# Optimization experiments

Hardware: AMD Instinct MI355X
Metric: run time of the kernel (lower is better)

The kernel has to match this reference:

```python
import jax, jax.numpy as jnp
import numpy as np

NUM_HEADS = 16
HEAD_DIM = 64  # hidden_size // num_heads = 1024 // 16


def setup_inputs() -> dict:
    key = jax.random.key(0)
    ks = jax.random.split(key, 5)
    B, S, D = 4, 2048, 1024
    scale = 1.0 / np.sqrt(D)
    return {
        "hidden_states": jax.random.normal(ks[0], (B, S, D), dtype=jnp.float32),
        "Wq": jax.random.normal(ks[1], (D, D), dtype=jnp.float32) * scale,
        "Wk": jax.random.normal(ks[2], (D, D), dtype=jnp.float32) * scale,
        "Wv": jax.random.normal(ks[3], (D, D), dtype=jnp.float32) * scale,
        "Wo": jax.random.normal(ks[4], (D, D), dtype=jnp.float32) * scale,
    }


def reference(hidden_states, Wq, Wk, Wv, Wo):
    B, S, D = hidden_states.shape
    H, hd = NUM_HEADS, HEAD_DIM
    # torch nn.Linear(y = x @ W.T), bias=False
    q = (hidden_states @ Wq.T).reshape(B, S, H, hd)
    k = (hidden_states @ Wk.T).reshape(B, S, H, hd)
    v = (hidden_states @ Wv.T).reshape(B, S, H, hd)
    q = q / jnp.sqrt(jnp.float32(hd))
    # scores: [B, H, S, S] — module materializes full score matrix
    scores = jnp.einsum("bqhd,bkhd->bhqk", q, k)
    weights = jax.nn.softmax(scores, axis=-1)
    attn = jnp.einsum("bhqk,bkhd->bqhd", weights, v).reshape(B, S, D)
    return attn @ Wo.T
```

## Files before the change

### kernel.cpp

```cpp
#include <hip/hip_runtime.h>

using u16 = unsigned short;
using u32 = unsigned int;
typedef __attribute__((ext_vector_type(8))) short bf16x8;
typedef __attribute__((ext_vector_type(4))) short bf16x4;
typedef __attribute__((ext_vector_type(4))) float f32x4;
typedef __attribute__((ext_vector_type(16))) float f32x16;
typedef __attribute__((ext_vector_type(4))) u32 u32x4;

__device__ __forceinline__ u16 f2bf(float f) {
  u32 u = __builtin_bit_cast(u32, f);
  u += 0x7FFFu + ((u >> 16) & 1u);
  return (u16)(u >> 16);
}

__device__ __forceinline__ void load_lds16(const void* g, void* l) {
  typedef const __attribute__((address_space(1))) u32 GA;
  typedef __attribute__((address_space(3))) u32 LA;
  __builtin_amdgcn_global_load_lds((GA*)g, (LA*)l, 16, 0, 0);
}

__device__ __forceinline__ bf16x4 tr16(const u16* p) {
  typedef __attribute__((address_space(3))) const u16 LT;
  bf16x4 d;
  asm volatile("ds_read_b64_tr_b16 %0, %1" : "=v"(d) : "v"((LT*)p));
  return d;
}

__device__ __forceinline__ float exp2_fast(float x) {
  float r;
  asm("v_exp_f32 %0, %1" : "=v"(r) : "v"(x));
  return r;
}

__device__ __forceinline__ u32 cvt_pk_bf16(float lo, float hi) {
  u32 r;
  asm("v_cvt_pk_bf16_f32 %0, %1, %2" : "=v"(r) : "v"(lo), "v"(hi));
  return r;
}

__device__ __forceinline__ void permlane32_swap(u32& a, u32& b) {
  asm volatile("v_permlane32_swap_b32 %0, %1" : "+v"(a), "+v"(b));
}

__global__ void cvt_bf16(const float* __restrict__ src, u16* __restrict__ dst,
                         int n4, float scale) {
  int i = blockIdx.x * blockDim.x + threadIdx.x;
  if (i >= n4) return;
  float4 v = reinterpret_cast<const float4*>(src)[i];
  ushort4 o;
  o.x = f2bf(v.x * scale);
  o.y = f2bf(v.y * scale);
  o.z = f2bf(v.z * scale);
  o.w = f2bf(v.w * scale);
  reinterpret_cast<ushort4*>(dst)[i] = o;
}

__global__ void cvt_w4(const float* __restrict__ Wq, const float* __restrict__ Wk,
                       const float* __restrict__ Wv, const float* __restrict__ Wo,
                       u16* __restrict__ dst, int n4seg, float qscale) {
  int i = blockIdx.x * blockDim.x + threadIdx.x;
  int seg = i / n4seg, off = i - seg * n4seg;
  const float* src = seg == 0 ? Wq : seg == 1 ? Wk : seg == 2 ? Wv : Wo;
  float sc = seg == 0 ? qscale : 1.0f;
  float4 v = reinterpret_cast<const float4*>(src)[off];
  ushort4 o;
  o.x = f2bf(v.x * sc);
  o.y = f2bf(v.y * sc);
  o.z = f2bf(v.z * sc);
  o.w = f2bf(v.w * sc);
  reinterpret_cast<ushort4*>(dst)[i] = o;
}

template <int NH>
__device__ __forceinline__ void mq(f32x4 (&acc)[4][4], bf16x8 (&afr)[4][2],
                                   bf16x8 (&bfr)[2][2]) {
  __builtin_amdgcn_s_setprio(1);
#pragma unroll
  for (int m = 0; m < 4; ++m)
#pragma unroll
    for (int n = 0; n < 2; ++n)
#pragma unroll
      for (int ks = 0; ks < 2; ++ks)
        acc[m][NH * 2 + n] = __builtin_amdgcn_mfma_f32_16x16x32_bf16(
            afr[m][ks], bfr[n][ks], acc[m][NH * 2 + n], 0, 0, 0);
  __builtin_amdgcn_s_setprio(0);
}

#define GBAR() __builtin_amdgcn_s_barrier()
#define PW()                                               \
  do {                                                     \
    GBAR();                                                \
    asm volatile("s_waitcnt lgkmcnt(0)" ::: "memory");     \
  } while (0)
#define PWV(N)                                                          \
  do {                                                                  \
    GBAR();                                                             \
    asm volatile("s_waitcnt vmcnt(" #N ") lgkmcnt(0)" ::: "memory");    \
  } while (0)

template <typename OutT>
__global__ __launch_bounds__(512, 2) void gemm256x128(
    const u16* __restrict__ A, const u16* __restrict__ Bw,
    OutT* __restrict__ C, int M, int N, int K) {
  __shared__ __align__(16) char ldsb[98304];
  const int tid = threadIdx.x;
  const int wid = tid >> 6, lane = tid & 63;
  const int wr = wid >> 1, wc = wid & 1;
  const int laneR = lane & 15, laneG = lane >> 4;
  const int swzR = (laneR & 7) << 4;

  const int nbm = M >> 8;
  const int cpx = gridDim.x >> 3;
  const int id = blockIdx.x;
  const int swzid = (id & 7) * cpx + (id >> 3);
  const int bm = swzid % nbm, bn = swzid / nbm;

  const u16* Ab = A + (size_t)(bm * 256) * K;
  const u16* Bb = Bw + (size_t)(bn * 128) * K;

  const int s_r = tid >> 3;
  const int s_k = ((tid & 7) ^ (s_r & 7)) * 8;

  auto stage_unit = [&](const u16* Xb, int dstoff, int row0, int kt) {
    char* d = ldsb + dstoff + wid * 1024;
#pragma unroll
    for (int j = 0; j < 2; ++j)
      load_lds16(Xb + (size_t)(row0 + j * 64 + s_r) * K + kt * 64 + s_k,
                 d + j * 8192);
  };
  auto rdA = [&](int buf, int m, int ks) -> bf16x8 {
    return *(const bf16x8*)(ldsb + buf * 32768 + (wr >> 1) * 16384 +
                            ((wr & 1) * 64 + m * 16 + laneR) * 128 +
                            ((ks * 64 + laneG * 16) ^ swzR));
  };
  auto rdB = [&](int buf, int nh, int n, int ks) -> bf16x8 {
    return *(const bf16x8*)(ldsb + 65536 + buf * 16384 +
                            (wc * 64 + nh * 32 + n * 16 + laneR) * 128 +
                            ((ks * 64 + laneG * 16) ^ swzR));
  };

  f32x4 acc[4][4];
#pragma unroll
  for (int i = 0; i < 4; ++i)
#pragma unroll
    for (int j = 0; j < 4; ++j) acc[i][j] = f32x4{0.f, 0.f, 0.f, 0.f};

  bf16x8 afr[4][2], bfr[2][2];
  auto readA = [&](int buf) {
#pragma unroll
    for (int m = 0; m < 4; ++m) {
      afr[m][0] = rdA(buf, m, 0);
      afr[m][1] = rdA(buf, m, 1);
    }
  };
  auto readB = [&](int buf, int nh) {
#pragma unroll
    for (int n = 0; n < 2; ++n) {
      bfr[n][0] = rdB(buf, nh, n, 0);
      bfr[n][1] = rdB(buf, nh, n, 1);
    }
  };

  const int NT = K >> 6, NI = K >> 7;

  stage_unit(Ab, 0, 0, 0);
  stage_unit(Ab, 16384, 128, 0);
  stage_unit(Bb, 65536, 0, 0);
  stage_unit(Ab, 32768, 0, 1);
  asm volatile("s_waitcnt vmcnt(2)" ::: "memory");
  GBAR();

  for (int i = 0; i < NI; ++i) {
    const int tb = (2 * i + 1) & (NT - 1);
    const int tc = (2 * i + 2) & (NT - 1);
    const int td = (2 * i + 3) & (NT - 1);
    readA(0); readB(0, 0);
    stage_unit(Ab, 32768 + 16384, 128, tb);
    stage_unit(Bb, 65536 + 16384, 0, tb);
    PW();
    mq<0>(acc, afr, bfr); GBAR();
    readB(0, 1);
    stage_unit(Ab, 0, 0, tc);
    stage_unit(Ab, 16384, 128, tc);
    PWV(4);
    mq<1>(acc, afr, bfr); GBAR();
    readA(1); readB(1, 0);
    stage_unit(Bb, 65536, 0, tc);
    PW();
    mq<0>(acc, afr, bfr); GBAR();
    readB(1, 1);
    stage_unit(Ab, 32768, 0, td);
    PWV(2);
    mq<1>(acc, afr, bfr); GBAR();
  }

  const int crow = bm * 256 + wr * 64;
  const int ccol = bn * 128 + wc * 64;
#pragma unroll
  for (int mf = 0; mf < 4; ++mf)
#pragma unroll
    for (int nf = 0; nf < 4; ++nf)
#pragma unroll
      for (int r = 0; r < 4; ++r) {
        int row = crow + mf * 16 + laneG * 4 + r;
        int col = ccol + nf * 16 + laneR;
        float v = acc[mf][nf][r];
        if constexpr (sizeof(OutT) == 2)
          C[(size_t)row * N + col] = f2bf(v);
        else
          C[(size_t)row * N + col] = v;
      }
}

__global__ __launch_bounds__(512, 4) void flash_attn(
    const u16* __restrict__ QKV, u16* __restrict__ O) {
  constexpr int S = 2048, DQ = 3072, DO = 1024;
  __shared__ u16 Kt[2][4096];
  __shared__ u16 Vt[2][4096];
  const int tid = threadIdx.x, wid = tid >> 6, lane = tid & 63;
  const int lq = lane & 31, hi = lane >> 5;

  const int id = blockIdx.x;
  const int jj0 = id >> 3;
  const int bh = (id & 7) * 8 + (jj0 >> 3), qt = jj0 & 7;
  const int b = bh >> 4, h = bh & 15;

  const size_t bq = (size_t)b * S * DQ;
  const u16* Qg = QKV + bq + h * 64;
  const u16* Kg = QKV + bq + 1024 + h * 64;
  const u16* Vg = QKV + bq + 2048 + h * 64;
  const int qrow0 = qt * 256 + wid * 32;

  const int k_kv = tid >> 3;
  const int k_col = ((tid & 7) ^ (k_kv & 7)) * 8;
  const int v_kv = ((tid >> 5) << 2) | ((tid >> 1) & 3);
  const int v_hd = (((tid >> 3) & 3) << 4) | ((tid & 1) << 3);

  bf16x8 qf[4];
#pragma unroll
  for (int kc = 0; kc < 4; ++kc)
    qf[kc] = *(const bf16x8*)&Qg[(size_t)(qrow0 + lq) * DQ + kc * 16 + hi * 8];

  f32x16 o0, o1;
#pragma unroll
  for (int r = 0; r < 16; ++r) { o0[r] = 0.f; o1[r] = 0.f; }
  float l = 0.f;

  auto stage = [&](int buf, int kv0) {
    load_lds16(Kg + (size_t)(kv0 + k_kv) * DQ + k_col, &Kt[buf][wid * 512]);
    load_lds16(Vg + (size_t)(kv0 + v_kv) * DQ + v_hd, &Vt[buf][wid * 512]);
  };

  stage(0, 0);
  __syncthreads();

  for (int t = 0; t < 32; ++t) {
    const int cur = t & 1;
    stage(cur ^ 1, ((t + 1) & 31) * 64);

    f32x16 st[2];
#pragma unroll
    for (int blk = 0; blk < 2; ++blk) {
#pragma unroll
      for (int r = 0; r < 16; ++r) st[blk][r] = 0.f;
      bf16x8 kf[4];
#pragma unroll
      for (int kc = 0; kc < 4; ++kc) {
        int kv = blk * 32 + lq;
        int byt = kv * 128 + ((kc * 32 + hi * 16) ^ ((kv & 7) << 4));
        kf[kc] = *(const bf16x8*)((const char*)&Kt[cur][0] + byt);
      }
      __builtin_amdgcn_s_setprio(1);
#pragma unroll
      for (int kc = 0; kc < 4; ++kc)
        st[blk] = __builtin_amdgcn_mfma_f32_32x32x16_bf16(kf[kc], qf[kc], st[blk], 0, 0, 0);
      __builtin_amdgcn_s_setprio(0);
    }

    float ps = 0.f;
#pragma unroll
    for (int blk = 0; blk < 2; ++blk)
#pragma unroll
      for (int r = 0; r < 16; ++r) {
        float p = exp2_fast(st[blk][r]);
        st[blk][r] = p;
        ps += p;
      }
    l += ps;

    u32 W0[8], W1[8];
#pragma unroll
    for (int r2 = 0; r2 < 8; ++r2) {
      W0[r2] = cvt_pk_bf16(st[0][2 * r2], st[0][2 * r2 + 1]);
      W1[r2] = cvt_pk_bf16(st[1][2 * r2], st[1][2 * r2 + 1]);
    }
    bf16x8 pb[4];
#pragma unroll
    for (int ks = 0; ks < 2; ++ks) {
      u32 a0 = W0[4 * ks], a2 = W0[4 * ks + 2];
      u32 a1 = W0[4 * ks + 1], a3 = W0[4 * ks + 3];
      permlane32_swap(a0, a2);
      permlane32_swap(a1, a3);
      pb[ks] = __builtin_bit_cast(bf16x8, u32x4{a0, a1, a2, a3});
    }
#pragma unroll
    for (int ks = 0; ks < 2; ++ks) {
      u32 a0 = W1[4 * ks], a2 = W1[4 * ks + 2];
      u32 a1 = W1[4 * ks + 1], a3 = W1[4 * ks + 3];
      permlane32_swap(a0, a2);
      permlane32_swap(a1, a3);
      pb[2 + ks] = __builtin_bit_cast(bf16x8, u32x4{a0, a1, a2, a3});
    }

#pragma unroll
    for (int c2 = 0; c2 < 2; ++c2) {
      bf16x4 vh[4][2];
      const int hb = c2 * 2 + ((lane >> 4) & 1);
#pragma unroll
      for (int ks = 0; ks < 4; ++ks)
#pragma unroll
        for (int p2 = 0; p2 < 2; ++p2) {
          int a = ks * 4 + hi * 2 + p2;
          vh[ks][p2] = tr16(&Vt[cur][(a * 4 + hb) * 64 + (lane & 15) * 4]);
        }
      asm volatile("s_waitcnt lgkmcnt(0)" ::: "memory");
      __builtin_amdgcn_sched_barrier(0);
      __builtin_amdgcn_s_setprio(1);
      f32x16 oc = c2 ? o1 : o0;
#pragma unroll
      for (int ks = 0; ks < 4; ++ks) {
        bf16x8 vf = __builtin_shufflevector(vh[ks][0], vh[ks][1], 0, 1, 2, 3, 4, 5, 6, 7);
        oc = __builtin_amdgcn_mfma_f32_32x32x16_bf16(vf, pb[ks], oc, 0, 0, 0);
      }
      if (c2) o1 = oc; else o0 = oc;
      __builtin_amdgcn_s_setprio(0);
    }

    __syncthreads();
  }

  l += __shfl_xor(l, 32);
  const float inv = 1.0f / l;
  const size_t boo = (size_t)b * S * DO + h * 64;
  const size_t qb = boo + (size_t)(qrow0 + lq) * DO;
#pragma unroll
  for (int r = 0; r < 16; ++r) {
    int hd = (r & 3) + 8 * (r >> 2) + 4 * hi;
    O[qb + hd] = f2bf(o0[r] * inv);
    O[qb + 32 + hd] = f2bf(o1[r] * inv);
  }
}

extern "C" void kernel_launch(void* const* d_in, const int* in_sizes, int n_in,
                              void* d_out, int out_size, void* d_ws, size_t ws_size,
                              hipStream_t stream) {
  const float* hs = (const float*)d_in[0];
  const float* Wq = (const float*)d_in[1];
  const float* Wk = (const float*)d_in[2];
  const float* Wv = (const float*)d_in[3];
  const float* Wo = (const float*)d_in[4];
  float* out = (float*)d_out;

  constexpr int Bn = 4, S = 2048, Dm = 1024;
  constexpr int M = Bn * S;
  constexpr size_t SZ = (size_t)M * Dm;
  constexpr size_t WSZ = (size_t)Dm * Dm;

  u16* wsp = (u16*)d_ws;
  u16* QKVb = wsp;
  u16* hs16 = QKVb + (size_t)M * 3072;
  u16* Ob = hs16;
  u16* W16 = hs16 + SZ;
  u16* Wo16 = W16 + 3 * WSZ;
  (void)ws_size; (void)in_sizes; (void)n_in; (void)out_size;

  cvt_bf16<<<(int)(SZ / 4 / 256), 256, 0, stream>>>(hs, hs16, (int)(SZ / 4), 1.0f);
  cvt_w4<<<(int)(4 * WSZ / 4 / 256), 256, 0, stream>>>(
      Wq, Wk, Wv, Wo, W16, (int)(WSZ / 4), 0.125f * 1.44269504f);

  gemm256x128<u16><<<(M / 256) * (3072 / 128), 512, 0, stream>>>(hs16, W16, QKVb, M, 3072, Dm);

  flash_attn<<<512, 512, 0, stream>>>(QKVb, Ob);

  gemm256x128<float><<<(M / 256) * (Dm / 128), 512, 0, stream>>>(Ob, Wo16, out, M, Dm, Dm);
}
```

Measured before the change: 197.1 us.

## Fuse conversion kernels, chunk GEMM tile order, triple-buffer attention K/V

Merges the activation and weight bf16 conversion kernels into one launch. Remaps GEMM block IDs into row/column chunks for better L2 reuse. The attention kernel moves from double- to triple-buffered K/V staging with prefetch two tiles ahead, waiting on vmcnt instead of a full syncthreads. It also seeds the first MFMA with a zero accumulator and drops the setprio hints. In exchange it uses more LDS per block and adds some scheduling risk.

```diff
diff --git a/kernel.cpp b/kernel.cpp
--- a/kernel.cpp
+++ b/kernel.cpp
@@ -43,34 +43,50 @@
   asm volatile("v_permlane32_swap_b32 %0, %1" : "+v"(a), "+v"(b));
 }
 
-__global__ void cvt_bf16(const float* __restrict__ src, u16* __restrict__ dst,
-                         int n4, float scale) {
+__global__ void cvt_all(const float* __restrict__ hs, const float* __restrict__ Wq,
+                        const float* __restrict__ Wk, const float* __restrict__ Wv,
+                        const float* __restrict__ Wo, u16* __restrict__ hs16,
+                        u16* __restrict__ w16, int hs4, int w4seg, float qscale) {
   int i = blockIdx.x * blockDim.x + threadIdx.x;
-  if (i >= n4) return;
-  float4 v = reinterpret_cast<const float4*>(src)[i];
-  ushort4 o;
-  o.x = f2bf(v.x * scale);
-  o.y = f2bf(v.y * scale);
-  o.z = f2bf(v.z * scale);
-  o.w = f2bf(v.w * scale);
-  reinterpret_cast<ushort4*>(dst)[i] = o;
-}
-
-__global__ void cvt_w4(const float* __restrict__ Wq, const float* __restrict__ Wk,
-                       const float* __restrict__ Wv, const float* __restrict__ Wo,
-                       u16* __restrict__ dst, int n4seg, float qscale) {
-  int i = blockIdx.x * blockDim.x + threadIdx.x;
-  int seg = i / n4seg, off = i - seg * n4seg;
-  const float* src = seg == 0 ? Wq : seg == 1 ? Wk : seg == 2 ? Wv : Wo;
-  float sc = seg == 0 ? qscale : 1.0f;
+  const float* src;
+  u16* dst;
+  float sc = 1.0f;
+  int off;
+  if (i < hs4) {
+    src = hs; dst = hs16; off = i;
+  } else {
+    int j = i - hs4;
+    int seg = j / w4seg;
+    off = j - seg * w4seg;
+    dst = w16 + (size_t)seg * (size_t)w4seg * 4;
+    src = seg == 0 ? Wq : seg == 1 ? Wk : seg == 2 ? Wv : Wo;
+    if (seg == 0) sc = qscale;
+  }
   float4 v = reinterpret_cast<const float4*>(src)[off];
   ushort4 o;
   o.x = f2bf(v.x * sc);
   o.y = f2bf(v.y * sc);
   o.z = f2bf(v.z * sc);
   o.w = f2bf(v.w * sc);
-  reinterpret_cast<ushort4*>(dst)[i] = o;
-}
+  reinterpret_cast<ushort4*>(dst)[off] = o;
+}
+
+#define GBAR() __builtin_amdgcn_s_barrier()
+#define PWAIT()                                            \
+  do {                                                     \
+    GBAR();                                                \
+    asm volatile("s_waitcnt lgkmcnt(0)" ::: "memory");     \
+  } while (0)
+#define PWAITV()                                                    \
+  do {                                                              \
+    GBAR();                                                         \
+    asm volatile("s_waitcnt vmcnt(2) lgkmcnt(0)" ::: "memory");     \
+  } while (0)
+#define PWAITV4()                                                   \
+  do {                                                              \
+    GBAR();                                                         \
+    asm volatile("s_waitcnt vmcnt(4) lgkmcnt(0)" ::: "memory");     \
+  } while (0)
 
 template <int NH>
 __device__ __forceinline__ void mq(f32x4 (&acc)[4][4], bf16x8 (&afr)[4][2],
@@ -87,22 +103,10 @@
   __builtin_amdgcn_s_setprio(0);
 }
 
-#define GBAR() __builtin_amdgcn_s_barrier()
-#define PW()                                               \
-  do {                                                     \
-    GBAR();                                                \
-    asm volatile("s_waitcnt lgkmcnt(0)" ::: "memory");     \
-  } while (0)
-#define PWV(N)                                                          \
-  do {                                                                  \
-    GBAR();                                                             \
-    asm volatile("s_waitcnt vmcnt(" #N ") lgkmcnt(0)" ::: "memory");    \
-  } while (0)
-
 template <typename OutT>
 __global__ __launch_bounds__(512, 2) void gemm256x128(
     const u16* __restrict__ A, const u16* __restrict__ Bw,
-    OutT* __restrict__ C, int M, int N, int K) {
+    OutT* __restrict__ C, int M, int N, int K, int rpc, int nbnc) {
   __shared__ __align__(16) char ldsb[98304];
   const int tid = threadIdx.x;
   const int wid = tid >> 6, lane = tid & 63;
@@ -110,11 +114,15 @@
   const int laneR = lane & 15, laneG = lane >> 4;
   const int swzR = (laneR & 7) << 4;
 
-  const int nbm = M >> 8;
+  const int nbn = N >> 7;
   const int cpx = gridDim.x >> 3;
   const int id = blockIdx.x;
   const int swzid = (id & 7) * cpx + (id >> 3);
-  const int bm = swzid % nbm, bn = swzid / nbm;
+  const int c = swzid / cpx, j = swzid % cpx;
+  const int ncc = nbn / nbnc;
+  const int chunk_row = c / ncc, chunk_col = c % ncc;
+  const int bm = chunk_row * rpc + j / nbnc;
+  const int bn = chunk_col * nbnc + j % nbnc;
 
   const u16* Ab = A + (size_t)(bm * 256) * K;
   const u16* Bb = Bw + (size_t)(bn * 128) * K;
@@ -125,9 +133,9 @@
   auto stage_unit = [&](const u16* Xb, int dstoff, int row0, int kt) {
     char* d = ldsb + dstoff + wid * 1024;
 #pragma unroll
-    for (int j = 0; j < 2; ++j)
-      load_lds16(Xb + (size_t)(row0 + j * 64 + s_r) * K + kt * 64 + s_k,
-                 d + j * 8192);
+    for (int jj = 0; jj < 2; ++jj)
+      load_lds16(Xb + (size_t)(row0 + jj * 64 + s_r) * K + kt * 64 + s_k,
+                 d + jj * 8192);
   };
   auto rdA = [&](int buf, int m, int ks) -> bf16x8 {
     return *(const bf16x8*)(ldsb + buf * 32768 + (wr >> 1) * 16384 +
@@ -144,7 +152,7 @@
 #pragma unroll
   for (int i = 0; i < 4; ++i)
 #pragma unroll
-    for (int j = 0; j < 4; ++j) acc[i][j] = f32x4{0.f, 0.f, 0.f, 0.f};
+    for (int jj = 0; jj < 4; ++jj) acc[i][jj] = f32x4{0.f, 0.f, 0.f, 0.f};
 
   bf16x8 afr[4][2], bfr[2][2];
   auto readA = [&](int buf) {
@@ -178,20 +186,20 @@
     readA(0); readB(0, 0);
     stage_unit(Ab, 32768 + 16384, 128, tb);
     stage_unit(Bb, 65536 + 16384, 0, tb);
-    PW();
+    PWAIT();
     mq<0>(acc, afr, bfr); GBAR();
     readB(0, 1);
     stage_unit(Ab, 0, 0, tc);
     stage_unit(Ab, 16384, 128, tc);
-    PWV(4);
+    PWAITV4();
     mq<1>(acc, afr, bfr); GBAR();
     readA(1); readB(1, 0);
     stage_unit(Bb, 65536, 0, tc);
-    PW();
+    PWAIT();
     mq<0>(acc, afr, bfr); GBAR();
     readB(1, 1);
     stage_unit(Ab, 32768, 0, td);
-    PWV(2);
+    PWAITV();
     mq<1>(acc, afr, bfr); GBAR();
   }
 
@@ -216,8 +224,8 @@
 __global__ __launch_bounds__(512, 4) void flash_attn(
     const u16* __restrict__ QKV, u16* __restrict__ O) {
   constexpr int S = 2048, DQ = 3072, DO = 1024;
-  __shared__ u16 Kt[2][4096];
-  __shared__ u16 Vt[2][4096];
+  __shared__ u16 Kt[3][4096];
+  __shared__ u16 Vt[3][4096];
   const int tid = threadIdx.x, wid = tid >> 6, lane = tid & 63;
   const int lq = lane & 31, hi = lane >> 5;
 
@@ -247,23 +255,28 @@
   for (int r = 0; r < 16; ++r) { o0[r] = 0.f; o1[r] = 0.f; }
   float l = 0.f;
 
+  f32x16 zz;
+#pragma unroll
+  for (int r = 0; r < 16; ++r) zz[r] = 0.f;
+
   auto stage = [&](int buf, int kv0) {
     load_lds16(Kg + (size_t)(kv0 + k_kv) * DQ + k_col, &Kt[buf][wid * 512]);
     load_lds16(Vg + (size_t)(kv0 + v_kv) * DQ + v_hd, &Vt[buf][wid * 512]);
   };
 
   stage(0, 0);
-  __syncthreads();
-
+  stage(1, 64);
+  asm volatile("s_waitcnt vmcnt(2)" ::: "memory");
+  __builtin_amdgcn_s_barrier();
+  asm volatile("" ::: "memory");
+
+  int cur = 0, pre = 2;
   for (int t = 0; t < 32; ++t) {
-    const int cur = t & 1;
-    stage(cur ^ 1, ((t + 1) & 31) * 64);
+    stage(pre, ((t + 2) & 31) * 64);
 
     f32x16 st[2];
 #pragma unroll
     for (int blk = 0; blk < 2; ++blk) {
-#pragma unroll
-      for (int r = 0; r < 16; ++r) st[blk][r] = 0.f;
       bf16x8 kf[4];
 #pragma unroll
       for (int kc = 0; kc < 4; ++kc) {
@@ -271,11 +284,10 @@
         int byt = kv * 128 + ((kc * 32 + hi * 16) ^ ((kv & 7) << 4));
         kf[kc] = *(const bf16x8*)((const char*)&Kt[cur][0] + byt);
       }
-      __builtin_amdgcn_s_setprio(1);
-#pragma unroll
-      for (int kc = 0; kc < 4; ++kc)
+      st[blk] = __builtin_amdgcn_mfma_f32_32x32x16_bf16(kf[0], qf[0], zz, 0, 0, 0);
+#pragma unroll
+      for (int kc = 1; kc < 4; ++kc)
         st[blk] = __builtin_amdgcn_mfma_f32_32x32x16_bf16(kf[kc], qf[kc], st[blk], 0, 0, 0);
-      __builtin_amdgcn_s_setprio(0);
     }
 
     float ps = 0.f;
@@ -326,7 +338,6 @@
         }
       asm volatile("s_waitcnt lgkmcnt(0)" ::: "memory");
       __builtin_amdgcn_sched_barrier(0);
-      __builtin_amdgcn_s_setprio(1);
       f32x16 oc = c2 ? o1 : o0;
 #pragma unroll
       for (int ks = 0; ks < 4; ++ks) {
@@ -334,10 +345,14 @@
         oc = __builtin_amdgcn_mfma_f32_32x32x16_bf16(vf, pb[ks], oc, 0, 0, 0);
       }
       if (c2) o1 = oc; else o0 = oc;
-      __builtin_amdgcn_s_setprio(0);
-    }
-
-    __syncthreads();
+    }
+
+    asm volatile("s_waitcnt vmcnt(2)" ::: "memory");
+    __builtin_amdgcn_s_barrier();
+    asm volatile("" ::: "memory");
+
+    cur = (cur == 2) ? 0 : cur + 1;
+    pre = (pre == 2) ? 0 : pre + 1;
   }
 
   l += __shfl_xor(l, 32);
@@ -375,13 +390,16 @@
   u16* Wo16 = W16 + 3 * WSZ;
   (void)ws_size; (void)in_sizes; (void)n_in; (void)out_size;
 
-  cvt_bf16<<<(int)(SZ / 4 / 256), 256, 0, stream>>>(hs, hs16, (int)(SZ / 4), 1.0f);
-  cvt_w4<<<(int)(4 * WSZ / 4 / 256), 256, 0, stream>>>(
-      Wq, Wk, Wv, Wo, W16, (int)(WSZ / 4), 0.125f * 1.44269504f);
-
-  gemm256x128<u16><<<(M / 256) * (3072 / 128), 512, 0, stream>>>(hs16, W16, QKVb, M, 3072, Dm);
+  constexpr int HS4 = (int)(SZ / 4);
+  constexpr int W4SEG = (int)(WSZ / 4);
+  cvt_all<<<(HS4 + 4 * W4SEG) / 256, 256, 0, stream>>>(
+      hs, Wq, Wk, Wv, Wo, hs16, W16, HS4, W4SEG, 0.125f * 1.44269504f);
+
+  gemm256x128<u16><<<(M / 256) * (3072 / 128), 512, 0, stream>>>(
+      hs16, W16, QKVb, M, 3072, Dm, 8, 12);
 
   flash_attn<<<512, 512, 0, stream>>>(QKVb, Ob);
 
-  gemm256x128<float><<<(M / 256) * (Dm / 128), 512, 0, stream>>>(Ob, Wo16, out, M, Dm, Dm);
-}
+  gemm256x128<float><<<(M / 256) * (Dm / 128), 512, 0, stream>>>(
+      Ob, Wo16, out, M, Dm, Dm, 4, 8);
+}
```

Result: faster. 179.1 us (-9.1%).
